# Kernel tuning notes

Hardware: AMD Instinct MI355X
Metric: run time of the kernel (lower is better)

## Reference

```python
import jax, jax.numpy as jnp
import numpy as np

N, D, DO, R, E, NV, K = 50000, 256, 256, 4, 500000, 10000, 8
EPS = 1e-8  # torch cosine_similarity eps


def setup_inputs() -> dict:
    key = jax.random.key(0)
    ks = jax.random.split(key, 7)
    x = jax.random.normal(ks[0], (N, D), jnp.float32)
    We = jax.random.normal(ks[1], (R, D, DO), jnp.float32) * (1.0 / np.sqrt(D))
    Wn = jax.random.normal(ks[2], (D, DO), jnp.float32) * (1.0 / np.sqrt(D))
    bn = jnp.zeros((DO,), jnp.float32)
    src = jax.random.randint(ks[3], (R, E), 0, N, jnp.int32)
    dst = jax.random.randint(ks[4], (R, E), 0, N, jnp.int32)
    candidates = jax.random.randint(ks[5], (NV, K), 0, NV, jnp.int32)
    return {"x": x, "We": We, "Wn": Wn, "bn": bn,
            "src": src, "dst": dst, "candidates": candidates, "n_vul": NV}


def reference(x, We, Wn, bn, src, dst, candidates, n_vul):
    n = x.shape[0]
    ht = x @ Wn + bn  # nweight projection (dst features) [N, DO]
    h_list, ma_list = [], []
    for r in range(We.shape[0]):  # small fixed set of relation types
        hr = x @ We[r]            # eweight projection, no bias [N, DO]
        hsrc = hr[src[r]]         # gather per-edge src features [E, DO]
        hdst = ht[dst[r]]         # gather per-edge dst features [E, DO]
        # cosine similarity edge attention
        num = jnp.sum(hsrc * hdst, axis=-1)
        den = (jnp.maximum(jnp.linalg.norm(hsrc, axis=-1), EPS)
               * jnp.maximum(jnp.linalg.norm(hdst, axis=-1), EPS))
        s = num / den             # [E]
        # reduce: h = sum_e a*h_src ; ma = mean_e a  (per dst node)
        hsum = jax.ops.segment_sum(s[:, None] * hsrc, dst[r], num_segments=n)
        asum = jax.ops.segment_sum(s, dst[r], num_segments=n)
        cnt = jax.ops.segment_sum(jnp.ones_like(s), dst[r], num_segments=n)
        ma_list.append(asum / jnp.maximum(cnt, 1.0))
        h_list.append(hsum)
    h = jnp.stack(h_list, axis=1)    # 'stack' cross-reducer -> [N, R, DO]
    ma = jnp.stack(ma_list, axis=1)  # [N, R]

    # AggregateLayer.edge_mask: pairwise candidate masking on entity ('vul') nodes
    Hv = h[:n_vul]                         # [NV, R, DO]
    diff = Hv[:, None] - Hv[candidates]    # [NV, K, R, DO]
    d2 = diff * diff
    att = jax.nn.softmax(-jnp.sqrt(jnp.sum(d2, axis=(2, 3))), axis=1)  # [NV, K]
    mask = jnp.exp(-jnp.einsum('nk,nkrd->nrd', att, d2))               # [NV, R, DO]
    h = jnp.concatenate([Hv * mask, h[n_vul:]], axis=0)

    # relation-axis softmax aggregation
    w = jax.nn.softmax(ma, axis=1)
    return jnp.einsum('nr,nrd->nd', w, h)  # [N, DO]
```

## Files before the change

kernel.cpp:

```cpp
#include <hip/hip_runtime.h>

#define N_NODES 50000
#define DIM     256
#define R_REL   4
#define E_EDGES 500000
#define NV_VUL  10000
#define K_CAND  8
#define EPS_C   1e-8f
#define RN      (R_REL * N_NODES)
#define NB      196
#define TB      (R_REL * NB)
#define BCAP    5120
#define EPB     4096
#define PREP_W   80
#define PREP_X   128
#define PREP_BIN ((R_REL * E_EDGES + EPB - 1) / EPB)

typedef short bf16x8 __attribute__((ext_vector_type(8)));
typedef float f32x4  __attribute__((ext_vector_type(4)));
typedef float f32x2  __attribute__((ext_vector_type(2)));
typedef unsigned short us8 __attribute__((ext_vector_type(8)));
typedef unsigned int u32x4 __attribute__((ext_vector_type(4)));

__device__ __forceinline__ unsigned short f2bf_rne(float f) {
  unsigned u = __builtin_bit_cast(unsigned, f);
  unsigned r = (u + 0x7FFFu + ((u >> 16) & 1u)) >> 16;
  return (unsigned short)r;
}
__device__ __forceinline__ float bf2f(unsigned short h) {
  unsigned u = ((unsigned)h) << 16;
  return __builtin_bit_cast(float, u);
}
__device__ __forceinline__ f32x2 expand_bf2(unsigned dw) {
  f32x2 v;
  v.x = __builtin_bit_cast(float, dw << 16);
  v.y = __builtin_bit_cast(float, dw & 0xFFFF0000u);
  return v;
}

__global__ __launch_bounds__(1024) void k_prep(const float* __restrict__ x,
                                               const float* __restrict__ Wn,
                                               const float* __restrict__ We,
                                               unsigned short* __restrict__ x16,
                                               short* __restrict__ Bthi,
                                               const int* __restrict__ src,
                                               const int* __restrict__ dst,
                                               int* __restrict__ cursor,
                                               int* __restrict__ binned) {
  __shared__ float tile[64][65];
  __shared__ int hist[TB];
  __shared__ int base[TB];
  int blk = blockIdx.x;
  int tid = threadIdx.x;

  if (blk < PREP_W) {
    int w   = blk / 16;
    int rem = blk % 16;
    int k0  = (rem / 4) * 64, n0 = (rem % 4) * 64;
    const float* W = (w == 0) ? Wn : We + (size_t)(w - 1) * 65536;
    int tx = tid & 63, ty = tid >> 6;
    for (int i = ty; i < 64; i += 16)
      tile[i][tx] = W[(size_t)(k0 + i) * 256 + n0 + tx];
    __syncthreads();
    for (int i = ty; i < 64; i += 16) {
      float f = tile[tx][i];
      size_t o = (size_t)w * 65536 + (size_t)(n0 + i) * 256 + k0 + tx;
      Bthi[o] = (short)f2bf_rne(f);
    }
    return;
  }
  if (blk < PREP_W + PREP_X) {
    const int total = N_NODES * DIM / 8;
    for (int i = (blk - PREP_W) * 1024 + tid; i < total; i += PREP_X * 1024) {
      float4 a = *(const float4*)(x + (size_t)i * 8);
      float4 b = *(const float4*)(x + (size_t)i * 8 + 4);
      us8 o;
      o[0] = f2bf_rne(a.x); o[1] = f2bf_rne(a.y); o[2] = f2bf_rne(a.z); o[3] = f2bf_rne(a.w);
      o[4] = f2bf_rne(b.x); o[5] = f2bf_rne(b.y); o[6] = f2bf_rne(b.z); o[7] = f2bf_rne(b.w);
      *(us8*)(x16 + (size_t)i * 8) = o;
    }
    return;
  }
  int bb = blk - PREP_W - PREP_X;
  for (int i = tid; i < TB; i += 1024) hist[i] = 0;
  __syncthreads();
  int e0 = bb * EPB;
  int myb[4], myrank[4], myp[4];
#pragma unroll
  for (int i = 0; i < 4; i++) {
    int e = e0 + i * 1024 + tid;
    myb[i] = -1;
    if (e < R_REL * E_EDGES) {
      int r = e / E_EDGES;
      int d = dst[e];
      int s = src[e];
      int b = r * NB + (d >> 8);
      myb[i]    = b;
      myp[i]    = (s << 8) | (d & 255);
      myrank[i] = atomicAdd(&hist[b], 1);
    }
  }
  __syncthreads();
  for (int i = tid; i < TB; i += 1024) {
    int c = hist[i];
    base[i] = c ? atomicAdd(&cursor[i], c) : 0;
  }
  __syncthreads();
#pragma unroll
  for (int i = 0; i < 4; i++) {
    if (myb[i] >= 0) {
      int pos = base[myb[i]] + myrank[i];
      if (pos < BCAP) binned[(size_t)myb[i] * BCAP + pos] = myp[i];
    }
  }
}

#define GBM 128
#define GBK 32
__global__ __launch_bounds__(512) void k_gemm_all(const unsigned short* __restrict__ A16,
                                                  const short* __restrict__ Bthi_all,
                                                  const float* __restrict__ bnb,
                                                  unsigned short* __restrict__ ht16,
                                                  unsigned short* __restrict__ hr0,
                                                  unsigned short* __restrict__ hr1,
                                                  unsigned short* __restrict__ hr2,
                                                  unsigned short* __restrict__ hr3,
                                                  float* __restrict__ rn_all,
                                                  int M) {
  __shared__ short Ahi_s[128][GBK + 8];
  __shared__ short Bhi_s[256][GBK + 8];
  __shared__ float nsq_s[128];
  const int w = blockIdx.z;
  const short* Bthi = Bthi_all + (size_t)w * 65536;
  unsigned short* C16 = (w == 0) ? ht16 : (w == 1) ? hr0 : (w == 2) ? hr1 : (w == 3) ? hr2 : hr3;
  const float* bias = (w == 0) ? bnb : nullptr;
  float* rn = rn_all + (size_t)w * N_NODES;

  const int t    = threadIdx.x;
  const int bm0  = blockIdx.x * GBM;
  const int wave = t >> 6, lane = t & 63;
  const int wm   = (wave >> 2) * 64;
  const int wn   = (wave & 3) * 64;
  const int m16  = lane & 15, kg = lane >> 4;

  if (t < 128) nsq_s[t] = 0.f;

  f32x4 acc[4][4] = {};

  const int arow = t >> 2, ac = t & 3;
  int agrow = bm0 + arow; if (agrow >= M) agrow = M - 1;
  const unsigned short* aptr = A16 + (size_t)agrow * 256 + ac * 8;
  const int brow0 = t >> 2, bc = t & 3;

  for (int k0 = 0; k0 < DIM; k0 += GBK) {
    *(us8*)&Ahi_s[arow][ac * 8] = *(const us8*)(aptr + k0);
    *(bf16x8*)&Bhi_s[brow0][bc * 8] =
        *(const bf16x8*)(Bthi + (size_t)brow0 * 256 + k0 + bc * 8);
    *(bf16x8*)&Bhi_s[brow0 + 128][bc * 8] =
        *(const bf16x8*)(Bthi + (size_t)(brow0 + 128) * 256 + k0 + bc * 8);
    __syncthreads();

    bf16x8 ah[4], bh[4];
#pragma unroll
    for (int i = 0; i < 4; i++) {
      ah[i] = *(const bf16x8*)&Ahi_s[wm + i * 16 + m16][kg * 8];
      bh[i] = *(const bf16x8*)&Bhi_s[wn + i * 16 + m16][kg * 8];
    }
#pragma unroll
    for (int mi = 0; mi < 4; mi++)
#pragma unroll
      for (int ni = 0; ni < 4; ni++)
        acc[mi][ni] = __builtin_amdgcn_mfma_f32_16x16x32_bf16(ah[mi], bh[ni], acc[mi][ni], 0, 0, 0);
    __syncthreads();
  }

#pragma unroll
  for (int mi = 0; mi < 4; mi++) {
    float ps[4] = {0.f, 0.f, 0.f, 0.f};
#pragma unroll
    for (int ni = 0; ni < 4; ni++) {
      int col = wn + ni * 16 + m16;
      float bb = bias ? bias[col] : 0.f;
      f32x4 v = acc[mi][ni];
#pragma unroll
      for (int j = 0; j < 4; j++) {
        float vj = v[j] + bb;
        int row = bm0 + wm + mi * 16 + kg * 4 + j;
        if (row < M) C16[(size_t)row * 256 + col] = f2bf_rne(vj);
        ps[j] += vj * vj;
      }
    }
#pragma unroll
    for (int j = 0; j < 4; j++) {
      float s = ps[j];
      s += __shfl_xor(s, 1);
      s += __shfl_xor(s, 2);
      s += __shfl_xor(s, 4);
      s += __shfl_xor(s, 8);
      if (m16 == 0) atomicAdd(&nsq_s[wm + mi * 16 + kg * 4 + j], s);
    }
  }
  __syncthreads();
  if (t < 128) {
    int row = bm0 + t;
    if (row < M) rn[row] = fminf(rsqrtf(nsq_s[t]), 1e8f);
  }
}

__global__ __launch_bounds__(1024) void k_bucket_scan(const int* __restrict__ cnt,
                                                      int* __restrict__ bbase,
                                                      int* __restrict__ offsets) {
  __shared__ int s[1024];
  int tid = threadIdx.x;
  int v = (tid < TB) ? cnt[tid] : 0;
  s[tid] = v;
  __syncthreads();
  for (int off = 1; off < 1024; off <<= 1) {
    int t2 = (tid >= off) ? s[tid - off] : 0;
    __syncthreads();
    s[tid] += t2;
    __syncthreads();
  }
  if (tid < TB) bbase[tid] = s[tid] - v;
  if (tid == TB - 1) offsets[RN] = s[tid];
}

__global__ __launch_bounds__(256) void k_csr(const int* __restrict__ binned,
                                             const int* __restrict__ cnt_arr,
                                             const int* __restrict__ bbase,
                                             int* __restrict__ offsets,
                                             int* __restrict__ edge_src) {
  __shared__ int hist[256];
  __shared__ int excl[256];
  int b   = blockIdx.x;
  int tid = threadIdx.x;
  int cnt = cnt_arr[b]; if (cnt > BCAP) cnt = BCAP;
  int gbase = bbase[b];
  hist[tid] = 0;
  __syncthreads();
  const int* bp = binned + (size_t)b * BCAP;
  for (int i = tid; i < cnt; i += 256) atomicAdd(&hist[bp[i] & 255], 1);
  __syncthreads();
  int v = hist[tid];
  excl[tid] = v;
  __syncthreads();
  for (int off = 1; off < 256; off <<= 1) {
    int t2 = (tid >= off) ? excl[tid - off] : 0;
    __syncthreads();
    excl[tid] += t2;
    __syncthreads();
  }
  int ex = excl[tid] - v;
  int r = b / NB, bloc = b % NB;
  int node = bloc * 256 + tid;
  if (node < N_NODES) offsets[r * N_NODES + node] = gbase + ex;
  hist[tid] = gbase + ex;
  __syncthreads();
  for (int i = tid; i < cnt; i += 256) {
    int p = bp[i];
    int pos = atomicAdd(&hist[p & 255], 1);
    edge_src[pos] = p >> 8;
  }
}

__global__ __launch_bounds__(256) void k_aggregate_fused(
    const unsigned short* __restrict__ hr0, const unsigned short* __restrict__ hr1,
    const unsigned short* __restrict__ hr2, const unsigned short* __restrict__ hr3,
    const unsigned short* __restrict__ ht16, const float* __restrict__ rn,
    const int* __restrict__ offsets, const int* __restrict__ edge_src,
    unsigned short* __restrict__ h16, float* __restrict__ ma,
    float* __restrict__ out) {
  int n    = (int)((blockIdx.x * (size_t)blockDim.x + threadIdx.x) >> 6);
  int lane = threadIdx.x & 63;
  if (n >= N_NODES) return;
  int g = lane >> 4, l16 = lane & 15;

  const u32x4* htp = (const u32x4*)(ht16 + (size_t)n * DIM + l16 * 16);
  u32x4 hta = __builtin_nontemporal_load(htp);
  u32x4 htb = __builtin_nontemporal_load(htp + 1);
  float rd = rn[n];
  f32x2 rd2 = {rd, rd};
  f32x2 hd2[8];
  hd2[0] = expand_bf2(hta[0]) * rd2; hd2[1] = expand_bf2(hta[1]) * rd2;
  hd2[2] = expand_bf2(hta[2]) * rd2; hd2[3] = expand_bf2(hta[3]) * rd2;
  hd2[4] = expand_bf2(htb[0]) * rd2; hd2[5] = expand_bf2(htb[1]) * rd2;
  hd2[6] = expand_bf2(htb[2]) * rd2; hd2[7] = expand_bf2(htb[3]) * rd2;

  const unsigned short* hr = (g == 0) ? hr0 : (g == 1) ? hr1 : (g == 2) ? hr2 : hr3;
  const float* nq = rn + (size_t)(1 + g) * N_NODES;
  int b   = offsets[g * N_NODES + n];
  int end = offsets[g * N_NODES + n + 1];

  f32x2 acc2[8] = {};
  float asum = 0.f;

  auto loadslot = [&](int i, uint4& ua, uint4& ub, float& q) {
    if (i < end) {
      int sn = edge_src[i];
      const uint4* rp = (const uint4*)(hr + (size_t)sn * DIM + l16 * 16);
      ua = rp[0]; ub = rp[1];
      q  = nq[sn];
    }
  };
  auto consume = [&](uint4 ua, uint4 ub, float q, bool valid) {
    f32x2 hs2[8];
    hs2[0] = expand_bf2(ua.x); hs2[1] = expand_bf2(ua.y);
    hs2[2] = expand_bf2(ua.z); hs2[3] = expand_bf2(ua.w);
    hs2[4] = expand_bf2(ub.x); hs2[5] = expand_bf2(ub.y);
    hs2[6] = expand_bf2(ub.z); hs2[7] = expand_bf2(ub.w);
    f32x2 d2 = hs2[0] * hd2[0];
#pragma unroll
    for (int i = 1; i < 8; i++) d2 += hs2[i] * hd2[i];
    float num = d2.x + d2.y;
    num += __shfl_xor(num, 1);
    num += __shfl_xor(num, 2);
    num += __shfl_xor(num, 4);
    num += __shfl_xor(num, 8);
    float s = valid ? num * q : 0.f;
    f32x2 s2 = {s, s};
#pragma unroll
    for (int i = 0; i < 8; i++) acc2[i] += hs2[i] * s2;
    asum += s;
  };

  uint4 uaA = {0,0,0,0}, ubA = {0,0,0,0}, uaB = {0,0,0,0}, ubB = {0,0,0,0};
  float qA = 1.f, qB = 1.f;
  loadslot(b,     uaA, ubA, qA);
  loadslot(b + 1, uaB, ubB, qB);
  for (int i = b; i < end; i += 2) {
    uint4 uaC = {0,0,0,0}, ubC = {0,0,0,0}, uaD = {0,0,0,0}, ubD = {0,0,0,0};
    float qC = 1.f, qD = 1.f;
    loadslot(i + 2, uaC, ubC, qC);
    loadslot(i + 3, uaD, ubD, qD);
    consume(uaA, ubA, qA, true);
    consume(uaB, ubB, qB, (i + 1) < end);
    uaA = uaC; ubA = ubC; qA = qC;
    uaB = uaD; ubB = ubD; qB = qD;
  }

  float mymean = asum / fmaxf((float)(end - b), 1.0f);

  if (n < NV_VUL) {
    us8 o1, o2;
#pragma unroll
    for (int i = 0; i < 4; i++) {
      o1[2 * i]     = f2bf_rne(acc2[i].x);
      o1[2 * i + 1] = f2bf_rne(acc2[i].y);
      o2[2 * i]     = f2bf_rne(acc2[4 + i].x);
      o2[2 * i + 1] = f2bf_rne(acc2[4 + i].y);
    }
    unsigned short* hp = h16 + ((size_t)n * R_REL + g) * DIM + l16 * 16;
    *(us8*)hp       = o1;
    *(us8*)(hp + 8) = o2;
    if (l16 == 0) ma[n * R_REL + g] = mymean;
  } else {
    float a1 = __shfl_xor(mymean, 16);
    float a2 = __shfl_xor(mymean, 32);
    float a3 = __shfl_xor(mymean, 48);
    float mx = fmaxf(fmaxf(mymean, a1), fmaxf(a2, a3));
    float e0 = expf(mymean - mx);
    float denom = e0 + expf(a1 - mx) + expf(a2 - mx) + expf(a3 - mx);
    float w = e0 / denom;
    f32x2 o[8];
#pragma unroll
    for (int i = 0; i < 8; i++) {
      f32x2 v = acc2[i] * (f32x2){w, w};
      v.x += __shfl_xor(v.x, 16); v.x += __shfl_xor(v.x, 32);
      v.y += __shfl_xor(v.y, 16); v.y += __shfl_xor(v.y, 32);
      o[i] = v;
    }
    if (g == 0) {
      float* op = out + (size_t)n * 256 + l16 * 16;
      f32x4 v0 = {o[0].x, o[0].y, o[1].x, o[1].y};
      f32x4 v1 = {o[2].x, o[2].y, o[3].x, o[3].y};
      f32x4 v2 = {o[4].x, o[4].y, o[5].x, o[5].y};
      f32x4 v3 = {o[6].x, o[6].y, o[7].x, o[7].y};
      __builtin_nontemporal_store(v0, (f32x4*)(op + 0));
      __builtin_nontemporal_store(v1, (f32x4*)(op + 4));
      __builtin_nontemporal_store(v2, (f32x4*)(op + 8));
      __builtin_nontemporal_store(v3, (f32x4*)(op + 12));
    }
  }
}

__global__ __launch_bounds__(256) void k_vuln_combine(const unsigned short* __restrict__ h16,
                                                      const int* __restrict__ cand,
                                                      const float* __restrict__ ma,
                                                      float* __restrict__ out) {
  __shared__ float red[8][4];
  __shared__ float dist2s[8];
  __shared__ float sm[1024];
  int n   = blockIdx.x;
  int tid = threadIdx.x;
  ushort4 hb = *(const ushort4*)(h16 + (size_t)n * 1024 + tid * 4);
  float4 hv;
  hv.x = bf2f(hb.x); hv.y = bf2f(hb.y); hv.z = bf2f(hb.z); hv.w = bf2f(hb.w);
  float4 d2[8];
  int wid = tid >> 6, lane = tid & 63;
#pragma unroll
  for (int k = 0; k < 8; k++) {
    int c = cand[n * 8 + k];
    ushort4 cb = *(const ushort4*)(h16 + (size_t)c * 1024 + tid * 4);
    float4 df;
    df.x = hv.x - bf2f(cb.x); df.y = hv.y - bf2f(cb.y);
    df.z = hv.z - bf2f(cb.z); df.w = hv.w - bf2f(cb.w);
    d2[k].x = df.x * df.x; d2[k].y = df.y * df.y;
    d2[k].z = df.z * df.z; d2[k].w = df.w * df.w;
    float v = d2[k].x + d2[k].y + d2[k].z + d2[k].w;
    for (int off = 32; off; off >>= 1) v += __shfl_xor(v, off);
    if (lane == 0) red[k][wid] = v;
  }
  __syncthreads();
  if (tid < 32) {
    int k = tid >> 2, w2 = tid & 3;
    float v = red[k][w2];
    v += __shfl_xor(v, 1, 4);
    v += __shfl_xor(v, 2, 4);
    if (w2 == 0) dist2s[k] = v;
  }
  __syncthreads();
  float dk[8], mn = 1e30f;
#pragma unroll
  for (int k = 0; k < 8; k++) { dk[k] = sqrtf(dist2s[k]); mn = fminf(mn, dk[k]); }
  float se = 0.f, att[8];
#pragma unroll
  for (int k = 0; k < 8; k++) { att[k] = expf(mn - dk[k]); se += att[k]; }
  float inv = 1.f / se;
  float4 accv = {0.f, 0.f, 0.f, 0.f};
#pragma unroll
  for (int k = 0; k < 8; k++) {
    float a = att[k] * inv;
    accv.x += a * d2[k].x; accv.y += a * d2[k].y;
    accv.z += a * d2[k].z; accv.w += a * d2[k].w;
  }
  float m0 = ma[n * 4 + 0], m1 = ma[n * 4 + 1], m2 = ma[n * 4 + 2], m3 = ma[n * 4 + 3];
  float mx = fmaxf(fmaxf(m0, m1), fmaxf(m2, m3));
  float w0 = expf(m0 - mx), w1 = expf(m1 - mx), w2f = expf(m2 - mx), w3 = expf(m3 - mx);
  float winv = 1.f / (w0 + w1 + w2f + w3);
  float wr = (tid < 64) ? w0 : (tid < 128) ? w1 : (tid < 192) ? w2f : w3;
  float c = wr * winv;
  float4 o;
  o.x = c * hv.x * expf(-accv.x);
  o.y = c * hv.y * expf(-accv.y);
  o.z = c * hv.z * expf(-accv.z);
  o.w = c * hv.w * expf(-accv.w);
  *(float4*)&sm[tid * 4] = o;
  __syncthreads();
  if (tid < 256) {
    float v = sm[tid] + sm[256 + tid] + sm[512 + tid] + sm[768 + tid];
    __builtin_nontemporal_store(v, out + (size_t)n * 256 + tid);
  }
}

__global__ void k_fallback(float* __restrict__ out, int out_size, float wsmb) {
  int i = blockIdx.x * blockDim.x + threadIdx.x;
  if (i < out_size) out[i] = (i == 0) ? wsmb : 0.f;
}

extern "C" void kernel_launch(void* const* d_in, const int* in_sizes, int n_in,
                              void* d_out, int out_size, void* d_ws, size_t ws_size,
                              hipStream_t stream) {
  const float* x   = (const float*)d_in[0];
  const float* We  = (const float*)d_in[1];
  const float* Wn  = (const float*)d_in[2];
  const float* bnb = (const float*)d_in[3];
  const int* src   = (const int*)d_in[4];
  const int* dst   = (const int*)d_in[5];
  const int* cand  = (const int*)d_in[6];
  float* out = (float*)d_out;

  char* ws = (char*)d_ws;
  size_t off = 0;
  auto alloc = [&](size_t bytes) -> void* {
    void* p = ws + off;
    off += (bytes + 255) & ~(size_t)255;
    return p;
  };
  unsigned short* ht16        = (unsigned short*)alloc((size_t)N_NODES * DIM * 2);
  unsigned short* h16         = (unsigned short*)alloc((size_t)NV_VUL * R_REL * DIM * 2);
  float*          ma          = (float*)alloc((size_t)NV_VUL * R_REL * 4);
  float*          rn          = (float*)alloc((size_t)5 * N_NODES * 4);
  int*            bucket_cnt  = (int*)alloc((size_t)TB * 4);
  int*            bucket_base = (int*)alloc((size_t)TB * 4);
  int*            offsets     = (int*)alloc((size_t)(RN + 1) * 4);
  int*            edge_src    = (int*)alloc((size_t)R_REL * E_EDGES * 4);
  short*          Bthi        = (short*)alloc((size_t)5 * 65536 * 2);
  unsigned short* x16         = (unsigned short*)alloc((size_t)N_NODES * DIM * 2);
  unsigned short* hr0         = (unsigned short*)alloc((size_t)N_NODES * DIM * 2);
  unsigned short* hr1         = (unsigned short*)alloc((size_t)N_NODES * DIM * 2);
  unsigned short* hr2         = (unsigned short*)alloc((size_t)N_NODES * DIM * 2);
  unsigned short* hr3         = (unsigned short*)alloc((size_t)N_NODES * DIM * 2);
  size_t required = off;
  (void)in_sizes; (void)n_in;

  if (ws_size < required) {
    k_fallback<<<(out_size + 255) / 256, 256, 0, stream>>>(out, out_size,
                                                           (float)(ws_size >> 20));
    return;
  }

  int* binned = (int*)h16;

  hipMemsetAsync(bucket_cnt, 0, (size_t)TB * 4, stream);

  k_prep<<<PREP_W + PREP_X + PREP_BIN, 1024, 0, stream>>>(x, Wn, We, x16, Bthi,
                                                          src, dst, bucket_cnt, binned);
  k_bucket_scan<<<1, 1024, 0, stream>>>(bucket_cnt, bucket_base, offsets);
  k_csr<<<TB, 256, 0, stream>>>(binned, bucket_cnt, bucket_base, offsets, edge_src);

  dim3 gemm_grid((N_NODES + GBM - 1) / GBM, 1, 5);
  k_gemm_all<<<gemm_grid, 512, 0, stream>>>(x16, Bthi, bnb, ht16, hr0, hr1, hr2, hr3,
                                            rn, N_NODES);

  k_aggregate_fused<<<(N_NODES * 64 + 255) / 256, 256, 0, stream>>>(
      hr0, hr1, hr2, hr3, ht16, rn, offsets, edge_src, h16, ma, out);

  k_vuln_combine<<<NV_VUL, 256, 0, stream>>>(h16, cand, ma, out);
}
```

Before: 336.2 us.

## Fuse x-to-bf16 conversion into GEMM and reuse each A tile across all weights

Removes the separate bf16 conversion pass over x in the prep kernel. The GEMM now loads fp32 x directly, converts a 64-row tile into shared memory once, and loops over all five weight matrices, so A is read once instead of five times. This drops the x16 write and read and the extra grid slices. In exchange, blocks are smaller (64 rows, 256 threads) and loop serially over the weights, with B re-streamed from global/L2 for every block, which lowers per-block parallelism and MFMA density.

```diff
diff --git a/kernel.cpp b/kernel.cpp
--- a/kernel.cpp
+++ b/kernel.cpp
@@ -13,7 +13,6 @@
 #define BCAP    5120
 #define EPB     4096
 #define PREP_W   80
-#define PREP_X   128
 #define PREP_BIN ((R_REL * E_EDGES + EPB - 1) / EPB)
 
 typedef short bf16x8 __attribute__((ext_vector_type(8)));
@@ -37,11 +36,16 @@
   v.y = __builtin_bit_cast(float, dw & 0xFFFF0000u);
   return v;
 }
-
-__global__ __launch_bounds__(1024) void k_prep(const float* __restrict__ x,
-                                               const float* __restrict__ Wn,
+__device__ __forceinline__ bf16x8 cvt8hi(float4 a, float4 b) {
+  float f[8] = {a.x, a.y, a.z, a.w, b.x, b.y, b.z, b.w};
+  bf16x8 hh;
+#pragma unroll
+  for (int i = 0; i < 8; i++) hh[i] = (short)f2bf_rne(f[i]);
+  return hh;
+}
+
+__global__ __launch_bounds__(1024) void k_prep(const float* __restrict__ Wn,
                                                const float* __restrict__ We,
-                                               unsigned short* __restrict__ x16,
                                                short* __restrict__ Bthi,
                                                const int* __restrict__ src,
                                                const int* __restrict__ dst,
@@ -69,19 +73,7 @@
     }
     return;
   }
-  if (blk < PREP_W + PREP_X) {
-    const int total = N_NODES * DIM / 8;
-    for (int i = (blk - PREP_W) * 1024 + tid; i < total; i += PREP_X * 1024) {
-      float4 a = *(const float4*)(x + (size_t)i * 8);
-      float4 b = *(const float4*)(x + (size_t)i * 8 + 4);
-      us8 o;
-      o[0] = f2bf_rne(a.x); o[1] = f2bf_rne(a.y); o[2] = f2bf_rne(a.z); o[3] = f2bf_rne(a.w);
-      o[4] = f2bf_rne(b.x); o[5] = f2bf_rne(b.y); o[6] = f2bf_rne(b.z); o[7] = f2bf_rne(b.w);
-      *(us8*)(x16 + (size_t)i * 8) = o;
-    }
-    return;
-  }
-  int bb = blk - PREP_W - PREP_X;
+  int bb = blk - PREP_W;
   for (int i = tid; i < TB; i += 1024) hist[i] = 0;
   __syncthreads();
   int e0 = bb * EPB;
@@ -115,9 +107,9 @@
   }
 }
 
-#define GBM 128
+#define GR  64
 #define GBK 32
-__global__ __launch_bounds__(512) void k_gemm_all(const unsigned short* __restrict__ A16,
+__global__ __launch_bounds__(256) void k_gemm_all(const float* __restrict__ x,
                                                   const short* __restrict__ Bthi_all,
                                                   const float* __restrict__ bnb,
                                                   unsigned short* __restrict__ ht16,
@@ -127,83 +119,88 @@
                                                   unsigned short* __restrict__ hr3,
                                                   float* __restrict__ rn_all,
                                                   int M) {
-  __shared__ short Ahi_s[128][GBK + 8];
-  __shared__ short Bhi_s[256][GBK + 8];
-  __shared__ float nsq_s[128];
-  const int w = blockIdx.z;
-  const short* Bthi = Bthi_all + (size_t)w * 65536;
-  unsigned short* C16 = (w == 0) ? ht16 : (w == 1) ? hr0 : (w == 2) ? hr1 : (w == 3) ? hr2 : hr3;
-  const float* bias = (w == 0) ? bnb : nullptr;
-  float* rn = rn_all + (size_t)w * N_NODES;
-
+  __shared__ short A_s[GR][264];
+  __shared__ short B_s[256][40];
+  __shared__ float nsq_s[GR];
   const int t    = threadIdx.x;
-  const int bm0  = blockIdx.x * GBM;
-  const int wave = t >> 6, lane = t & 63;
-  const int wm   = (wave >> 2) * 64;
-  const int wn   = (wave & 3) * 64;
+  const int bm0  = blockIdx.x * GR;
+  const int lane = t & 63;
+  const int wn   = (t >> 6) * 64;
   const int m16  = lane & 15, kg = lane >> 4;
 
-  if (t < 128) nsq_s[t] = 0.f;
-
-  f32x4 acc[4][4] = {};
-
-  const int arow = t >> 2, ac = t & 3;
-  int agrow = bm0 + arow; if (agrow >= M) agrow = M - 1;
-  const unsigned short* aptr = A16 + (size_t)agrow * 256 + ac * 8;
-  const int brow0 = t >> 2, bc = t & 3;
-
-  for (int k0 = 0; k0 < DIM; k0 += GBK) {
-    *(us8*)&Ahi_s[arow][ac * 8] = *(const us8*)(aptr + k0);
-    *(bf16x8*)&Bhi_s[brow0][bc * 8] =
-        *(const bf16x8*)(Bthi + (size_t)brow0 * 256 + k0 + bc * 8);
-    *(bf16x8*)&Bhi_s[brow0 + 128][bc * 8] =
-        *(const bf16x8*)(Bthi + (size_t)(brow0 + 128) * 256 + k0 + bc * 8);
-    __syncthreads();
-
-    bf16x8 ah[4], bh[4];
-#pragma unroll
-    for (int i = 0; i < 4; i++) {
-      ah[i] = *(const bf16x8*)&Ahi_s[wm + i * 16 + m16][kg * 8];
-      bh[i] = *(const bf16x8*)&Bhi_s[wn + i * 16 + m16][kg * 8];
-    }
-#pragma unroll
-    for (int mi = 0; mi < 4; mi++)
-#pragma unroll
-      for (int ni = 0; ni < 4; ni++)
-        acc[mi][ni] = __builtin_amdgcn_mfma_f32_16x16x32_bf16(ah[mi], bh[ni], acc[mi][ni], 0, 0, 0);
-    __syncthreads();
-  }
-
-#pragma unroll
-  for (int mi = 0; mi < 4; mi++) {
-    float ps[4] = {0.f, 0.f, 0.f, 0.f};
-#pragma unroll
-    for (int ni = 0; ni < 4; ni++) {
-      int col = wn + ni * 16 + m16;
-      float bb = bias ? bias[col] : 0.f;
-      f32x4 v = acc[mi][ni];
+  for (int i = t; i < GR * 32; i += 256) {
+    int row = i >> 5, c = i & 31;
+    int gr = bm0 + row; if (gr >= M) gr = M - 1;
+    const float* xp = x + (size_t)gr * 256 + c * 8;
+    float4 a = *(const float4*)xp;
+    float4 b = *(const float4*)(xp + 4);
+    *(bf16x8*)&A_s[row][c * 8] = cvt8hi(a, b);
+  }
+
+  unsigned short* Cs[5] = {ht16, hr0, hr1, hr2, hr3};
+
+#pragma unroll 1
+  for (int w = 0; w < 5; w++) {
+    const short* Bthi = Bthi_all + (size_t)w * 65536;
+    unsigned short* C16 = Cs[w];
+    float* rn = rn_all + (size_t)w * N_NODES;
+
+    if (t < GR) nsq_s[t] = 0.f;
+    __syncthreads();
+
+    f32x4 acc[4][4] = {};
+    for (int k0 = 0; k0 < DIM; k0 += GBK) {
+      for (int i = t; i < 1024; i += 256) {
+        int n = i >> 2, c = i & 3;
+        *(bf16x8*)&B_s[n][c * 8] = *(const bf16x8*)(Bthi + (size_t)n * 256 + k0 + c * 8);
+      }
+      __syncthreads();
+
+      bf16x8 ah[4], bh[4];
+#pragma unroll
+      for (int i = 0; i < 4; i++) {
+        ah[i] = *(const bf16x8*)&A_s[i * 16 + m16][k0 + kg * 8];
+        bh[i] = *(const bf16x8*)&B_s[wn + i * 16 + m16][kg * 8];
+      }
+#pragma unroll
+      for (int mi = 0; mi < 4; mi++)
+#pragma unroll
+        for (int ni = 0; ni < 4; ni++)
+          acc[mi][ni] = __builtin_amdgcn_mfma_f32_16x16x32_bf16(ah[mi], bh[ni], acc[mi][ni], 0, 0, 0);
+      __syncthreads();
+    }
+
+#pragma unroll
+    for (int mi = 0; mi < 4; mi++) {
+      float ps[4] = {0.f, 0.f, 0.f, 0.f};
+#pragma unroll
+      for (int ni = 0; ni < 4; ni++) {
+        int col = wn + ni * 16 + m16;
+        float bb = (w == 0) ? bnb[col] : 0.f;
+        f32x4 v = acc[mi][ni];
+#pragma unroll
+        for (int j = 0; j < 4; j++) {
+          float vj = v[j] + bb;
+          int row = bm0 + mi * 16 + kg * 4 + j;
+          if (row < M) C16[(size_t)row * 256 + col] = f2bf_rne(vj);
+          ps[j] += vj * vj;
+        }
+      }
 #pragma unroll
       for (int j = 0; j < 4; j++) {
-        float vj = v[j] + bb;
-        int row = bm0 + wm + mi * 16 + kg * 4 + j;
-        if (row < M) C16[(size_t)row * 256 + col] = f2bf_rne(vj);
-        ps[j] += vj * vj;
+        float s = ps[j];
+        s += __shfl_xor(s, 1);
+        s += __shfl_xor(s, 2);
+        s += __shfl_xor(s, 4);
+        s += __shfl_xor(s, 8);
+        if (m16 == 0) atomicAdd(&nsq_s[mi * 16 + kg * 4 + j], s);
       }
     }
-#pragma unroll
-    for (int j = 0; j < 4; j++) {
-      float s = ps[j];
-      s += __shfl_xor(s, 1);
-      s += __shfl_xor(s, 2);
-      s += __shfl_xor(s, 4);
-      s += __shfl_xor(s, 8);
-      if (m16 == 0) atomicAdd(&nsq_s[wm + mi * 16 + kg * 4 + j], s);
-    }
-  }
-  __syncthreads();
-  if (t < 128) {
-    int row = bm0 + t;
-    if (row < M) rn[row] = fminf(rsqrtf(nsq_s[t]), 1e8f);
+    __syncthreads();
+    if (t < GR) {
+      int row = bm0 + t;
+      if (row < M) rn[row] = fminf(rsqrtf(nsq_s[t]), 1e8f);
+    }
   }
 }
 
@@ -485,7 +482,6 @@
   int*            offsets     = (int*)alloc((size_t)(RN + 1) * 4);
   int*            edge_src    = (int*)alloc((size_t)R_REL * E_EDGES * 4);
   short*          Bthi        = (short*)alloc((size_t)5 * 65536 * 2);
-  unsigned short* x16         = (unsigned short*)alloc((size_t)N_NODES * DIM * 2);
   unsigned short* hr0         = (unsigned short*)alloc((size_t)N_NODES * DIM * 2);
   unsigned short* hr1         = (unsigned short*)alloc((size_t)N_NODES * DIM * 2);
   unsigned short* hr2         = (unsigned short*)alloc((size_t)N_NODES * DIM * 2);
@@ -503,14 +499,13 @@
 
   hipMemsetAsync(bucket_cnt, 0, (size_t)TB * 4, stream);
 
-  k_prep<<<PREP_W + PREP_X + PREP_BIN, 1024, 0, stream>>>(x, Wn, We, x16, Bthi,
-                                                          src, dst, bucket_cnt, binned);
+  k_prep<<<PREP_W + PREP_BIN, 1024, 0, stream>>>(Wn, We, Bthi, src, dst,
+                                                 bucket_cnt, binned);
   k_bucket_scan<<<1, 1024, 0, stream>>>(bucket_cnt, bucket_base, offsets);
   k_csr<<<TB, 256, 0, stream>>>(binned, bucket_cnt, bucket_base, offsets, edge_src);
 
-  dim3 gemm_grid((N_NODES + GBM - 1) / GBM, 1, 5);
-  k_gemm_all<<<gemm_grid, 512, 0, stream>>>(x16, Bthi, bnb, ht16, hr0, hr1, hr2, hr3,
-                                            rn, N_NODES);
+  k_gemm_all<<<(N_NODES + GR - 1) / GR, 256, 0, stream>>>(x, Bthi, bnb, ht16,
+                                                          hr0, hr1, hr2, hr3, rn, N_NODES);
 
   k_aggregate_fused<<<(N_NODES * 64 + 255) / 256, 256, 0, stream>>>(
       hr0, hr1, hr2, hr3, ht16, rn, offsets, edge_src, h16, ma, out);
```

Result: slower. 419.6 us (+24.8%).

## Merge CSR build into GEMM launch and drop separate bucket scan kernel

Applied to the files above, without the earlier changes.

Removes the single-block bucket scan and the separate CSR kernel. CSR bucket blocks are appended to the GEMM grid, and each block computes its own global base by summing the preceding bucket counts. Two launches and one serial dependency go away, and the CSR work can overlap with GEMM blocks. In exchange, every CSR block does a redundant prefix sum of up to 784 counts, and the CSR blocks run at 512 threads with half of them idle during the scan. offsets[RN] is now a constant set to the total edge count instead of the scanned sum.

```diff
diff --git a/kernel.cpp b/kernel.cpp
--- a/kernel.cpp
+++ b/kernel.cpp
@@ -16,6 +16,11 @@
 #define PREP_X   128
 #define PREP_BIN ((R_REL * E_EDGES + EPB - 1) / EPB)
 
+#define GBM 128
+#define GBK 32
+#define GEMM_BLKS  ((N_NODES + GBM - 1) / GBM)
+#define GEMM_TOTAL (GEMM_BLKS * 5)
+
 typedef short bf16x8 __attribute__((ext_vector_type(8)));
 typedef float f32x4  __attribute__((ext_vector_type(4)));
 typedef float f32x2  __attribute__((ext_vector_type(2)));
@@ -115,9 +120,7 @@
   }
 }
 
-#define GBM 128
-#define GBK 32
-__global__ __launch_bounds__(512) void k_gemm_all(const unsigned short* __restrict__ A16,
+__global__ __launch_bounds__(512) void k_gemm_csr(const unsigned short* __restrict__ A16,
                                                   const short* __restrict__ Bthi_all,
                                                   const float* __restrict__ bnb,
                                                   unsigned short* __restrict__ ht16,
@@ -126,139 +129,141 @@
                                                   unsigned short* __restrict__ hr2,
                                                   unsigned short* __restrict__ hr3,
                                                   float* __restrict__ rn_all,
+                                                  const int* __restrict__ binned,
+                                                  const int* __restrict__ cnt_arr,
+                                                  int* __restrict__ offsets,
+                                                  int* __restrict__ edge_src,
                                                   int M) {
   __shared__ short Ahi_s[128][GBK + 8];
   __shared__ short Bhi_s[256][GBK + 8];
   __shared__ float nsq_s[128];
-  const int w = blockIdx.z;
-  const short* Bthi = Bthi_all + (size_t)w * 65536;
-  unsigned short* C16 = (w == 0) ? ht16 : (w == 1) ? hr0 : (w == 2) ? hr1 : (w == 3) ? hr2 : hr3;
-  const float* bias = (w == 0) ? bnb : nullptr;
-  float* rn = rn_all + (size_t)w * N_NODES;
-
-  const int t    = threadIdx.x;
-  const int bm0  = blockIdx.x * GBM;
-  const int wave = t >> 6, lane = t & 63;
-  const int wm   = (wave >> 2) * 64;
-  const int wn   = (wave & 3) * 64;
-  const int m16  = lane & 15, kg = lane >> 4;
-
-  if (t < 128) nsq_s[t] = 0.f;
-
-  f32x4 acc[4][4] = {};
-
-  const int arow = t >> 2, ac = t & 3;
-  int agrow = bm0 + arow; if (agrow >= M) agrow = M - 1;
-  const unsigned short* aptr = A16 + (size_t)agrow * 256 + ac * 8;
-  const int brow0 = t >> 2, bc = t & 3;
-
-  for (int k0 = 0; k0 < DIM; k0 += GBK) {
-    *(us8*)&Ahi_s[arow][ac * 8] = *(const us8*)(aptr + k0);
-    *(bf16x8*)&Bhi_s[brow0][bc * 8] =
-        *(const bf16x8*)(Bthi + (size_t)brow0 * 256 + k0 + bc * 8);
-    *(bf16x8*)&Bhi_s[brow0 + 128][bc * 8] =
-        *(const bf16x8*)(Bthi + (size_t)(brow0 + 128) * 256 + k0 + bc * 8);
+  __shared__ int hist2[256];
+  __shared__ int excl2[256];
+  __shared__ int wred[8];
+  const int blk = blockIdx.x;
+  const int t   = threadIdx.x;
+
+  if (blk < GEMM_TOTAL) {
+    const int w  = blk / GEMM_BLKS;
+    const int bx = blk % GEMM_BLKS;
+    const short* Bthi = Bthi_all + (size_t)w * 65536;
+    unsigned short* C16 = (w == 0) ? ht16 : (w == 1) ? hr0 : (w == 2) ? hr1 : (w == 3) ? hr2 : hr3;
+    const float* bias = (w == 0) ? bnb : nullptr;
+    float* rn = rn_all + (size_t)w * N_NODES;
+
+    const int bm0  = bx * GBM;
+    const int wave = t >> 6, lane = t & 63;
+    const int wm   = (wave >> 2) * 64;
+    const int wn   = (wave & 3) * 64;
+    const int m16  = lane & 15, kg = lane >> 4;
+
+    if (t < 128) nsq_s[t] = 0.f;
+
+    f32x4 acc[4][4] = {};
+
+    const int arow = t >> 2, ac = t & 3;
+    int agrow = bm0 + arow; if (agrow >= M) agrow = M - 1;
+    const unsigned short* aptr = A16 + (size_t)agrow * 256 + ac * 8;
+    const int brow0 = t >> 2, bc = t & 3;
+
+    for (int k0 = 0; k0 < DIM; k0 += GBK) {
+      *(us8*)&Ahi_s[arow][ac * 8] = *(const us8*)(aptr + k0);
+      *(bf16x8*)&Bhi_s[brow0][bc * 8] =
+          *(const bf16x8*)(Bthi + (size_t)brow0 * 256 + k0 + bc * 8);
+      *(bf16x8*)&Bhi_s[brow0 + 128][bc * 8] =
+          *(const bf16x8*)(Bthi + (size_t)(brow0 + 128) * 256 + k0 + bc * 8);
+      __syncthreads();
+
+      bf16x8 ah[4], bh[4];
+#pragma unroll
+      for (int i = 0; i < 4; i++) {
+        ah[i] = *(const bf16x8*)&Ahi_s[wm + i * 16 + m16][kg * 8];
+        bh[i] = *(const bf16x8*)&Bhi_s[wn + i * 16 + m16][kg * 8];
+      }
+#pragma unroll
+      for (int mi = 0; mi < 4; mi++)
+#pragma unroll
+        for (int ni = 0; ni < 4; ni++)
+          acc[mi][ni] = __builtin_amdgcn_mfma_f32_16x16x32_bf16(ah[mi], bh[ni], acc[mi][ni], 0, 0, 0);
+      __syncthreads();
+    }
+
+#pragma unroll
+    for (int mi = 0; mi < 4; mi++) {
+      float ps[4] = {0.f, 0.f, 0.f, 0.f};
+#pragma unroll
+      for (int ni = 0; ni < 4; ni++) {
+        int col = wn + ni * 16 + m16;
+        float bb = bias ? bias[col] : 0.f;
+        f32x4 v = acc[mi][ni];
+#pragma unroll
+        for (int j = 0; j < 4; j++) {
+          float vj = v[j] + bb;
+          int row = bm0 + wm + mi * 16 + kg * 4 + j;
+          if (row < M) C16[(size_t)row * 256 + col] = f2bf_rne(vj);
+          ps[j] += vj * vj;
+        }
+      }
+#pragma unroll
+      for (int j = 0; j < 4; j++) {
+        float s = ps[j];
+        s += __shfl_xor(s, 1);
+        s += __shfl_xor(s, 2);
+        s += __shfl_xor(s, 4);
+        s += __shfl_xor(s, 8);
+        if (m16 == 0) atomicAdd(&nsq_s[wm + mi * 16 + kg * 4 + j], s);
+      }
+    }
     __syncthreads();
-
-    bf16x8 ah[4], bh[4];
-#pragma unroll
-    for (int i = 0; i < 4; i++) {
-      ah[i] = *(const bf16x8*)&Ahi_s[wm + i * 16 + m16][kg * 8];
-      bh[i] = *(const bf16x8*)&Bhi_s[wn + i * 16 + m16][kg * 8];
-    }
-#pragma unroll
-    for (int mi = 0; mi < 4; mi++)
-#pragma unroll
-      for (int ni = 0; ni < 4; ni++)
-        acc[mi][ni] = __builtin_amdgcn_mfma_f32_16x16x32_bf16(ah[mi], bh[ni], acc[mi][ni], 0, 0, 0);
+    if (t < 128) {
+      int row = bm0 + t;
+      if (row < M) rn[row] = fminf(rsqrtf(nsq_s[t]), 1e8f);
+    }
+    return;
+  }
+
+  const int b = blk - GEMM_TOTAL;
+  int partial = 0;
+  for (int i = t; i < b; i += 512) partial += cnt_arr[i];
+  for (int off = 32; off; off >>= 1) partial += __shfl_xor(partial, off);
+  if ((t & 63) == 0) wred[t >> 6] = partial;
+  __syncthreads();
+  if (t == 0) {
+    int s = 0;
+#pragma unroll
+    for (int i = 0; i < 8; i++) s += wred[i];
+    wred[0] = s;
+    if (b == 0) offsets[RN] = R_REL * E_EDGES;
+  }
+  __syncthreads();
+  const int gbase = wred[0];
+
+  int cntb = cnt_arr[b]; if (cntb > BCAP) cntb = BCAP;
+  if (t < 256) hist2[t] = 0;
+  __syncthreads();
+  const int* bp = binned + (size_t)b * BCAP;
+  for (int i = t; i < cntb; i += 512) atomicAdd(&hist2[bp[i] & 255], 1);
+  __syncthreads();
+  int v = 0;
+  if (t < 256) { v = hist2[t]; excl2[t] = v; }
+  __syncthreads();
+  for (int off = 1; off < 256; off <<= 1) {
+    int t2 = (t < 256 && t >= off) ? excl2[t - off] : 0;
     __syncthreads();
-  }
-
-#pragma unroll
-  for (int mi = 0; mi < 4; mi++) {
-    float ps[4] = {0.f, 0.f, 0.f, 0.f};
-#pragma unroll
-    for (int ni = 0; ni < 4; ni++) {
-      int col = wn + ni * 16 + m16;
-      float bb = bias ? bias[col] : 0.f;
-      f32x4 v = acc[mi][ni];
-#pragma unroll
-      for (int j = 0; j < 4; j++) {
-        float vj = v[j] + bb;
-        int row = bm0 + wm + mi * 16 + kg * 4 + j;
-        if (row < M) C16[(size_t)row * 256 + col] = f2bf_rne(vj);
-        ps[j] += vj * vj;
-      }
-    }
-#pragma unroll
-    for (int j = 0; j < 4; j++) {
-      float s = ps[j];
-      s += __shfl_xor(s, 1);
-      s += __shfl_xor(s, 2);
-      s += __shfl_xor(s, 4);
-      s += __shfl_xor(s, 8);
-      if (m16 == 0) atomicAdd(&nsq_s[wm + mi * 16 + kg * 4 + j], s);
-    }
-  }
-  __syncthreads();
-  if (t < 128) {
-    int row = bm0 + t;
-    if (row < M) rn[row] = fminf(rsqrtf(nsq_s[t]), 1e8f);
-  }
-}
-
-__global__ __launch_bounds__(1024) void k_bucket_scan(const int* __restrict__ cnt,
-                                                      int* __restrict__ bbase,
-                                                      int* __restrict__ offsets) {
-  __shared__ int s[1024];
-  int tid = threadIdx.x;
-  int v = (tid < TB) ? cnt[tid] : 0;
-  s[tid] = v;
-  __syncthreads();
-  for (int off = 1; off < 1024; off <<= 1) {
-    int t2 = (tid >= off) ? s[tid - off] : 0;
+    if (t < 256) excl2[t] += t2;
     __syncthreads();
-    s[tid] += t2;
-    __syncthreads();
-  }
-  if (tid < TB) bbase[tid] = s[tid] - v;
-  if (tid == TB - 1) offsets[RN] = s[tid];
-}
-
-__global__ __launch_bounds__(256) void k_csr(const int* __restrict__ binned,
-                                             const int* __restrict__ cnt_arr,
-                                             const int* __restrict__ bbase,
-                                             int* __restrict__ offsets,
-                                             int* __restrict__ edge_src) {
-  __shared__ int hist[256];
-  __shared__ int excl[256];
-  int b   = blockIdx.x;
-  int tid = threadIdx.x;
-  int cnt = cnt_arr[b]; if (cnt > BCAP) cnt = BCAP;
-  int gbase = bbase[b];
-  hist[tid] = 0;
-  __syncthreads();
-  const int* bp = binned + (size_t)b * BCAP;
-  for (int i = tid; i < cnt; i += 256) atomicAdd(&hist[bp[i] & 255], 1);
-  __syncthreads();
-  int v = hist[tid];
-  excl[tid] = v;
-  __syncthreads();
-  for (int off = 1; off < 256; off <<= 1) {
-    int t2 = (tid >= off) ? excl[tid - off] : 0;
-    __syncthreads();
-    excl[tid] += t2;
-    __syncthreads();
-  }
-  int ex = excl[tid] - v;
-  int r = b / NB, bloc = b % NB;
-  int node = bloc * 256 + tid;
-  if (node < N_NODES) offsets[r * N_NODES + node] = gbase + ex;
-  hist[tid] = gbase + ex;
-  __syncthreads();
-  for (int i = tid; i < cnt; i += 256) {
+  }
+  if (t < 256) {
+    int ex = excl2[t] - v;
+    int r = b / NB, bloc = b % NB;
+    int node = bloc * 256 + t;
+    if (node < N_NODES) offsets[r * N_NODES + node] = gbase + ex;
+    hist2[t] = gbase + ex;
+  }
+  __syncthreads();
+  for (int i = t; i < cntb; i += 512) {
     int p = bp[i];
-    int pos = atomicAdd(&hist[p & 255], 1);
+    int pos = atomicAdd(&hist2[p & 255], 1);
     edge_src[pos] = p >> 8;
   }
 }
@@ -481,7 +486,6 @@
   float*          ma          = (float*)alloc((size_t)NV_VUL * R_REL * 4);
   float*          rn          = (float*)alloc((size_t)5 * N_NODES * 4);
   int*            bucket_cnt  = (int*)alloc((size_t)TB * 4);
-  int*            bucket_base = (int*)alloc((size_t)TB * 4);
   int*            offsets     = (int*)alloc((size_t)(RN + 1) * 4);
   int*            edge_src    = (int*)alloc((size_t)R_REL * E_EDGES * 4);
   short*          Bthi        = (short*)alloc((size_t)5 * 65536 * 2);
@@ -505,12 +509,11 @@
 
   k_prep<<<PREP_W + PREP_X + PREP_BIN, 1024, 0, stream>>>(x, Wn, We, x16, Bthi,
                                                           src, dst, bucket_cnt, binned);
-  k_bucket_scan<<<1, 1024, 0, stream>>>(bucket_cnt, bucket_base, offsets);
-  k_csr<<<TB, 256, 0, stream>>>(binned, bucket_cnt, bucket_base, offsets, edge_src);
-
-  dim3 gemm_grid((N_NODES + GBM - 1) / GBM, 1, 5);
-  k_gemm_all<<<gemm_grid, 512, 0, stream>>>(x16, Bthi, bnb, ht16, hr0, hr1, hr2, hr3,
-                                            rn, N_NODES);
+
+  k_gemm_csr<<<GEMM_TOTAL + TB, 512, 0, stream>>>(x16, Bthi, bnb, ht16,
+                                                  hr0, hr1, hr2, hr3, rn,
+                                                  binned, bucket_cnt, offsets, edge_src,
+                                                  N_NODES);
 
   k_aggregate_fused<<<(N_NODES * 64 + 255) / 256, 256, 0, stream>>>(
       hr0, hr1, hr2, hr3, ht16, rn, offsets, edge_src, h16, ma, out);
```

After: 324.9 us. 3.4% less time.
